# Kernel optimization log

Hardware: AMD Instinct MI355X
Metric: run time of the kernel (lower is better)

The kernel has to match this reference:

```python
import jax, jax.numpy as jnp
import numpy as np
from jax import lax

EPS = 1e-5      # BatchNorm1d default eps
SLOPE = 0.01    # LeakyReLU default negative_slope
DN = ('NCDHW', 'OIDHW', 'NCDHW')
PAD_31 = ((1, 1), (0, 0), (1, 1))   # kernel (3,1,3), padding (1,0,1)
PAD_13 = ((0, 0), (1, 1), (1, 1))   # kernel (1,3,3), padding (0,1,1)
PAD_P = ((1, 1), (1, 1), (1, 1))    # pool kernel 3, padding 1
STRIDE_P = (2, 2, 1)                # height_pooling=False -> stride (2,2,1)


def setup_inputs() -> dict:
    key = jax.random.key(0)
    ks = jax.random.split(key, 8)
    B, Cin, Cout = 1, 32, 64
    D1, D2, D3 = 160, 160, 32
    mask = jax.random.randint(ks[0], (B, 1, D1, D2, D3), 0, 2) > 0
    x = jax.random.normal(ks[1], (B, Cin, D1, D2, D3), dtype=jnp.float32)

    def w(k, cin, cout, kd, kh, kw):
        return jax.random.normal(k, (cout, cin, kd, kh, kw), dtype=jnp.float32) * 0.05

    inp = {
        'x': x, 'mask': mask,
        'W_A1': w(ks[2], Cin, Cout, 3, 1, 3),
        'W_A2': w(ks[3], Cout, Cout, 1, 3, 3),
        'W_B1': w(ks[4], Cin, Cout, 1, 3, 3),
        'W_B2': w(ks[5], Cout, Cout, 3, 1, 3),
        'W_pool': w(ks[6], Cout, Cout, 3, 3, 3),
    }
    for name in ('A1', 'A2', 'B1', 'B2'):
        inp['g_' + name] = jnp.ones((Cout,), jnp.float32)
        inp['b_' + name] = jnp.zeros((Cout,), jnp.float32)
    return inp


def _conv(h, W, pad, stride=(1, 1, 1)):
    return lax.conv_general_dilated(h, W, stride, pad, dimension_numbers=DN)


def _lrelu(h):
    return jnp.where(h >= 0, h, SLOPE * h)


def _masked_bn(h, m, n_active, gamma, beta):
    # BatchNorm1d over the [N_active, C] sparse feature tensor:
    # per-channel stats over active voxels only (biased variance, training mode).
    mean = jnp.sum(h * m, axis=(0, 2, 3, 4)) / n_active
    mu = mean[None, :, None, None, None]
    var = jnp.sum(((h - mu) ** 2) * m, axis=(0, 2, 3, 4)) / n_active
    inv = lax.rsqrt(var + EPS)[None, :, None, None, None]
    out = (h - mu) * inv * gamma[None, :, None, None, None] + beta[None, :, None, None, None]
    return out * m  # keep inactive sites exactly zero


def reference(x, mask, W_A1, W_A2, W_B1, W_B2, W_pool,
              g_A1, b_A1, g_A2, b_A2, g_B1, b_B1, g_B2, b_B2):
    m = mask.astype(x.dtype)                      # [B,1,D1,D2,D3] active-site indicator
    n_active = jnp.sum(m)
    xs = x * m                                    # sparse input: zero at inactive voxels

    def subm(h, W, pad):
        # submanifold conv: compute only at active output sites (same site set as input)
        return _conv(h, W, pad) * m

    # branch A: conv3x1 -> LeakyReLU -> BN -> conv1x3 -> LeakyReLU -> BN
    res_A = _masked_bn(_lrelu(subm(xs, W_A1, PAD_31)), m, n_active, g_A1, b_A1)
    res_A = _masked_bn(_lrelu(subm(res_A, W_A2, PAD_13)), m, n_active, g_A2, b_A2)

    # branch B: conv1x3 -> LeakyReLU -> BN -> conv3x1 -> LeakyReLU -> BN
    res_B = _masked_bn(_lrelu(subm(xs, W_B1, PAD_13)), m, n_active, g_B1, b_B1)
    res_B = _masked_bn(_lrelu(subm(res_B, W_B2, PAD_31)), m, n_active, g_B2, b_B2)

    res_B = res_B + res_A

    # strided SparseConv3d pool: output active where any input in 3x3x3 window is active
    ones_k = jnp.ones((1, 1, 3, 3, 3), x.dtype)
    out_mask = (_conv(m, ones_k, PAD_P, STRIDE_P) > 0).astype(x.dtype)
    down = _conv(res_B, W_pool, PAD_P, STRIDE_P) * out_mask
    return (down, res_B)
```

## Files before the change

### kernel.cpp

```cpp
#include <hip/hip_runtime.h>

static constexpr int ND1=160, ND2=160, ND3=32;
static constexpr int SP  = ND1*ND2*ND3;
static constexpr int CO  = 64;
static constexpr int OD1=80, OD2=80, OD3=32;
static constexpr int OSP = OD1*OD2*OD3;
static constexpr int NSC = 64;

typedef __attribute__((ext_vector_type(8))) short  short8;
typedef __attribute__((ext_vector_type(4))) float  f32x4;

__device__ __forceinline__ float b2f(unsigned u){ return __uint_as_float(u<<16); }
__device__ __forceinline__ unsigned short f2b(float f){
    unsigned u = __float_as_uint(f);
    u += 0x7fffu + ((u>>16)&1u);
    return (unsigned short)(u>>16);
}

__global__ void k_detect(const unsigned char* __restrict__ mb, int* __restrict__ flag)
{
    __shared__ int lf;
    if (threadIdx.x == 0) lf = 0;
    __syncthreads();
    int f = 0;
    for (int i = blockIdx.x*256 + threadIdx.x; i < SP; i += gridDim.x*256) {
        unsigned char b = mb[i];
        if (b > 1) f |= 4;
        if (b != 0 && (i & 3)) f |= 1;
    }
    if (f) atomicOr(&lf, f);
    __syncthreads();
    if (threadIdx.x == 0 && lf) atomicOr(flag, lf);
}

__global__ void k_mask(const void* __restrict__ mraw, const int* __restrict__ flag,
                       float* __restrict__ m, float* __restrict__ nactN)
{
    int i = blockIdx.x*256 + threadIdx.x;
    int f = *flag;
    float v;
    if (f & 4)      v = (reinterpret_cast<const float*>(mraw)[i] != 0.f) ? 1.f : 0.f;
    else if (f & 1) v = (reinterpret_cast<const unsigned char*>(mraw)[i] != 0) ? 1.f : 0.f;
    else            v = (reinterpret_cast<const int*>(mraw)[i] != 0) ? 1.f : 0.f;
    m[i] = v;
    float s = v;
    #pragma unroll
    for (int off = 32; off > 0; off >>= 1) s += __shfl_xor(s, off);
    __shared__ float wsum[4];
    if ((threadIdx.x & 63) == 0) wsum[threadIdx.x >> 6] = s;
    __syncthreads();
    if (threadIdx.x == 0) atomicAdd(&nactN[blockIdx.x & (NSC-1)], wsum[0]+wsum[1]+wsum[2]+wsum[3]);
}

__global__ void k_outmask(const float* __restrict__ m, float* __restrict__ om)
{
    int i = blockIdx.x*256 + threadIdx.x;
    int o3 = i & 31; int t = i >> 5; int o2 = t % OD2; int o1 = t / OD2;
    float s = 0.f;
    for (int kd = 0; kd < 3; kd++) { int d1 = 2*o1 - 1 + kd; if ((unsigned)d1 >= ND1) continue;
      for (int kh = 0; kh < 3; kh++) { int d2 = 2*o2 - 1 + kh; if ((unsigned)d2 >= ND2) continue;
        for (int kw = 0; kw < 3; kw++) { int d3 = o3 - 1 + kw; if ((unsigned)d3 >= ND3) continue;
          s += m[(d1*ND2 + d2)*ND3 + d3];
        } } }
    om[i] = (s > 0.f) ? 1.f : 0.f;
}

__global__ void k_finalize2(const float* __restrict__ SN0, const float* __restrict__ g0,
                            const float* __restrict__ b0, float* __restrict__ o0,
                            const float* __restrict__ SN1, const float* __restrict__ g1,
                            const float* __restrict__ b1, float* __restrict__ o1,
                            const float* __restrict__ nactN)
{
    const float* SN = blockIdx.x ? SN1 : SN0;
    const float* g  = blockIdx.x ? g1  : g0;
    const float* b  = blockIdx.x ? b1  : b0;
    float*       o  = blockIdx.x ? o1  : o0;
    int c = threadIdx.x;
    float s1 = 0.f, s2 = 0.f;
    #pragma unroll 4
    for (int k = 0; k < NSC; k++){
        s1 += SN[k*128 + c];
        s2 += SN[k*128 + 64 + c];
    }
    float nn = nactN[c];
    #pragma unroll
    for (int off = 32; off > 0; off >>= 1) nn += __shfl_xor(nn, off);
    float mean = s1 / nn;
    float var  = s2 / nn - mean*mean;
    float inv  = rsqrtf(var + 1e-5f);
    float sc   = inv * g[c];
    o[c]      = sc;
    o[64 + c] = b[c] - mean*sc;
}

__global__ void k_wprep(const float* __restrict__ W, unsigned short* __restrict__ Wt,
                        int CIN, int NT)
{
    int i = blockIdx.x*256 + threadIdx.x;
    int K = CIN*NT;
    if (i >= 64*K) return;
    int ksub = i & 31;
    int t = i >> 5;
    int co = t & 63;
    int kc = t >> 6;
    int nch = CIN >> 5;
    int tap = kc / nch;
    int ci  = (kc - tap*nch)*32 + ksub;
    Wt[i] = f2b(W[((size_t)co*CIN + ci)*NT + tap]);
}

__global__ void k_prep_x(const float* __restrict__ x, const float* __restrict__ m,
                         unsigned short* __restrict__ xt)
{
    __shared__ float t[64][33];
    int sp0 = blockIdx.x*64;
    int tid = threadIdx.x;
    int c = tid>>6, s = tid&63;
    float mm = m[sp0+s];
    #pragma unroll
    for (int r=0;r<8;r++){
        int ci = c + r*4;
        t[s][ci] = x[(size_t)ci*SP + sp0 + s]*mm;
    }
    __syncthreads();
    int sp = tid>>2, c0 = (tid&3)*8;
    unsigned short o[8];
    #pragma unroll
    for (int i=0;i<8;i++) o[i] = f2b(t[sp][c0+i]);
    uint4 pk;
    pk.x = o[0] | ((unsigned)o[1]<<16);
    pk.y = o[2] | ((unsigned)o[3]<<16);
    pk.z = o[4] | ((unsigned)o[5]<<16);
    pk.w = o[6] | ((unsigned)o[7]<<16);
    *reinterpret_cast<uint4*>(xt + (size_t)(sp0+sp)*32 + c0) = pk;
}

__global__ void k_resB(const unsigned short* __restrict__ hA, const unsigned short* __restrict__ hB,
                       const float* __restrict__ sA, const float* __restrict__ sB,
                       const float* __restrict__ m,
                       unsigned short* __restrict__ rbt, float* __restrict__ resf)
{
    __shared__ float t[64][65];
    __shared__ float ss[256];
    int tid = threadIdx.x;
    if (tid < 128){ ss[tid] = sA[tid]; ss[128+tid] = sB[tid]; }
    __syncthreads();
    int sp0 = blockIdx.x*64;
    int sp = tid>>2, c0 = (tid&3)*16;
    float mm = m[sp0+sp];
    const size_t base = (size_t)(sp0+sp)*64 + c0;
    uint4 a0 = *reinterpret_cast<const uint4*>(hA + base);
    uint4 a1 = *reinterpret_cast<const uint4*>(hA + base + 8);
    uint4 b0 = *reinterpret_cast<const uint4*>(hB + base);
    uint4 b1 = *reinterpret_cast<const uint4*>(hB + base + 8);
    unsigned ua[16] = {a0.x&0xffffu,a0.x>>16,a0.y&0xffffu,a0.y>>16,a0.z&0xffffu,a0.z>>16,a0.w&0xffffu,a0.w>>16,
                       a1.x&0xffffu,a1.x>>16,a1.y&0xffffu,a1.y>>16,a1.z&0xffffu,a1.z>>16,a1.w&0xffffu,a1.w>>16};
    unsigned ub[16] = {b0.x&0xffffu,b0.x>>16,b0.y&0xffffu,b0.y>>16,b0.z&0xffffu,b0.z>>16,b0.w&0xffffu,b0.w>>16,
                       b1.x&0xffffu,b1.x>>16,b1.y&0xffffu,b1.y>>16,b1.z&0xffffu,b1.z>>16,b1.w&0xffffu,b1.w>>16};
    unsigned short o[16];
    #pragma unroll
    for (int q=0;q<16;q++){
        int ci = c0+q;
        float v = (b2f(ua[q])*ss[ci] + ss[64+ci] + b2f(ub[q])*ss[128+ci] + ss[192+ci])*mm;
        t[sp][ci] = v;
        o[q] = f2b(v);
    }
    uint4 p0, p1;
    p0.x = o[0]|((unsigned)o[1]<<16);  p0.y = o[2]|((unsigned)o[3]<<16);
    p0.z = o[4]|((unsigned)o[5]<<16);  p0.w = o[6]|((unsigned)o[7]<<16);
    p1.x = o[8]|((unsigned)o[9]<<16);  p1.y = o[10]|((unsigned)o[11]<<16);
    p1.z = o[12]|((unsigned)o[13]<<16); p1.w = o[14]|((unsigned)o[15]<<16);
    *reinterpret_cast<uint4*>(rbt + base)     = p0;
    *reinterpret_cast<uint4*>(rbt + base + 8) = p1;
    __syncthreads();
    int ci = tid>>2, s0 = (tid&3)*16;
    #pragma unroll
    for (int kq=0;kq<4;kq++){
        float4 ov;
        ov.x = t[s0+4*kq+0][ci]; ov.y = t[s0+4*kq+1][ci];
        ov.z = t[s0+4*kq+2][ci]; ov.w = t[s0+4*kq+3][ci];
        *reinterpret_cast<float4*>(resf + (size_t)ci*SP + sp0 + s0 + 4*kq) = ov;
    }
}

template<int KIND, int CIN, bool HASAFF>
__launch_bounds__(256, (CIN==32) ? 3 : 2)
__global__ void mconv10(const unsigned short* __restrict__ in,
                        const unsigned short* __restrict__ Wt,
                        const float* __restrict__ scsh,
                        const float* __restrict__ mstage,
                        const float* __restrict__ mout,
                        unsigned short* __restrict__ outb,
                        float* __restrict__ statsN)
{
    constexpr int NCH  = CIN/32;
    constexpr int NKC  = NCH*9;
    constexpr int NR   = 10;
    constexpr int ROWB = 34*CIN*2;
    constexpr int SWZ  = (CIN==64) ? 7 : 3;
    __shared__ __align__(16) char lds[NR*ROWB];
    __shared__ float sst[128];

    const int tid = threadIdx.x;
    const int w = tid>>6, l = tid&63, g = l>>4, lj = l&15;
    const int h = w&1, rg = w>>1;

    int gi = (blockIdx.x & 7)*(gridDim.x>>3) + (blockIdx.x>>3);
    int z  = gi % 160;
    int r0 = (gi / 160)*8;

    if (tid < 128) sst[tid] = 0.f;

    const int sd3 = tid>>3;
    const int k0  = (tid&7)*(CIN/8);

    float sc[8], sh[8];
    if (HASAFF){
        #pragma unroll
        for (int j=0;j<8;j++){ sc[j]=scsh[k0+j]; sh[j]=scsh[64+k0+j]; }
    }

    for (int i = tid; i < NR*2*(CIN/8); i += 256){
        int per = CIN/8;
        int rr = i / (2*per);
        int rem = i - rr*2*per;
        int slot = (rem >= per) ? 33 : 0;
        int kc16 = (rem >= per) ? (rem - per) : rem;
        int dst = rr*ROWB + slot*CIN*2 + kc16*16;
        dst ^= ((slot&SWZ)<<4);
        *reinterpret_cast<uint4*>(lds + dst) = make_uint4(0,0,0,0);
    }

    if (CIN==64){
        uint4 v[NR]; float mmr[NR];
        #pragma unroll
        for (int rr=0; rr<NR; rr++){
            int rw = r0 - 1 + rr;
            v[rr] = make_uint4(0,0,0,0); mmr[rr] = 0.f;
            if ((unsigned)rw < 160u){
                int vox = (KIND==0) ? ((rw*ND2 + z)*ND3 + sd3)
                                    : ((z*ND2 + rw)*ND3 + sd3);
                v[rr] = *reinterpret_cast<const uint4*>(in + (size_t)vox*CIN + k0);
                if (HASAFF) mmr[rr] = mstage[vox];
            }
        }
        #pragma unroll
        for (int rr=0; rr<NR; rr++){
            uint4 vv = v[rr];
            if (HASAFF){
                float mm = mmr[rr];
                unsigned us[8] = {vv.x&0xffffu,vv.x>>16,vv.y&0xffffu,vv.y>>16,
                                  vv.z&0xffffu,vv.z>>16,vv.w&0xffffu,vv.w>>16};
                unsigned short o[8];
                #pragma unroll
                for (int j=0;j<8;j++) o[j] = f2b((b2f(us[j])*sc[j]+sh[j])*mm);
                vv.x = o[0]|((unsigned)o[1]<<16); vv.y = o[2]|((unsigned)o[3]<<16);
                vv.z = o[4]|((unsigned)o[5]<<16); vv.w = o[6]|((unsigned)o[7]<<16);
            }
            int dst = (rr*ROWB + (((sd3+1)*CIN + k0)*2)) ^ (((sd3+1)&SWZ)<<4);
            *reinterpret_cast<uint4*>(lds + dst) = vv;
        }
    } else {
        uint2 v[NR];
        #pragma unroll
        for (int rr=0; rr<NR; rr++){
            int rw = r0 - 1 + rr;
            v[rr] = make_uint2(0,0);
            if ((unsigned)rw < 160u){
                int vox = (KIND==0) ? ((rw*ND2 + z)*ND3 + sd3)
                                    : ((z*ND2 + rw)*ND3 + sd3);
                v[rr] = *reinterpret_cast<const uint2*>(in + (size_t)vox*CIN + k0);
            }
        }
        #pragma unroll
        for (int rr=0; rr<NR; rr++){
            int dst = (rr*ROWB + (((sd3+1)*CIN + k0)*2)) ^ (((sd3+1)&SWZ)<<4);
            *reinterpret_cast<uint2*>(lds + dst) = v[rr];
        }
    }

    short8 pa[NKC][2];
    {
        const unsigned short* wb = Wt + (size_t)(h*32)*32 + lj*32 + g*8;
        #pragma unroll
        for (int kc=0; kc<NKC; kc++){
            pa[kc][0] = *reinterpret_cast<const short8*>(wb + (size_t)kc*2048);
            pa[kc][1] = *reinterpret_cast<const short8*>(wb + (size_t)kc*2048 + 512);
        }
    }

    int tb[8], ovox[8];
    float mm[8];
    #pragma unroll
    for (int t=0;t<8;t++){
        int rowb = rg*4 + (t>>1);
        int o3   = (t&1)*16 + lj;
        tb[t] = rowb*ROWB + ((o3*CIN + g*8)*2);
        int o2r = r0 + rowb;
        ovox[t] = (KIND==0) ? ((o2r*ND2 + z)*ND3 + o3)
                            : ((z*ND2 + o2r)*ND3 + o3);
        mm[t] = mout[ovox[t]];
    }
    int swz[3];
    #pragma unroll
    for (int kw=0;kw<3;kw++) swz[kw] = ((lj+kw)&SWZ)<<4;

    __syncthreads();

    f32x4 acc[2][8];
    #pragma unroll
    for (int c=0;c<2;c++)
        #pragma unroll
        for (int t=0;t<8;t++)
            #pragma unroll
            for (int q=0;q<4;q++) acc[c][t][q] = 0.f;

    #pragma unroll
    for (int ch=0; ch<NCH; ch++){
        #pragma unroll
        for (int tap=0; tap<9; tap++){
            const int kd = tap/3, kw = tap - kd*3;
            const int kc = tap*NCH + ch;
            const int tapoff = kd*ROWB + (kw*CIN + ch*32)*2;
            #pragma unroll
            for (int t=0;t<8;t++){
                int off = (tb[t] + tapoff) ^ swz[kw];
                short8 bv = *reinterpret_cast<const short8*>(lds + off);
                acc[0][t] = __builtin_amdgcn_mfma_f32_16x16x32_bf16(pa[kc][0], bv, acc[0][t], 0,0,0);
                acc[1][t] = __builtin_amdgcn_mfma_f32_16x16x32_bf16(pa[kc][1], bv, acc[1][t], 0,0,0);
            }
        }
    }

    #pragma unroll
    for (int c=0;c<2;c++){
        const int ct = h*2 + c;
        float s1[4] = {0.f,0.f,0.f,0.f};
        float s2[4] = {0.f,0.f,0.f,0.f};
        #pragma unroll
        for (int t=0;t<8;t++){
            float v[4];
            #pragma unroll
            for (int r=0;r<4;r++){
                float xv = acc[c][t][r]*mm[t];
                xv = (xv >= 0.f) ? xv : 0.01f*xv;
                v[r] = xv; s1[r] += xv; s2[r] += xv*xv;
            }
            unsigned lo = f2b(v[0]) | ((unsigned)f2b(v[1])<<16);
            unsigned hi = f2b(v[2]) | ((unsigned)f2b(v[3])<<16);
            *reinterpret_cast<uint2*>(outb + (size_t)ovox[t]*64 + ct*16 + g*4) = make_uint2(lo,hi);
        }
        #pragma unroll
        for (int r=0;r<4;r++){
            float a = s1[r], b = s2[r];
            a += __shfl_xor(a,1); b += __shfl_xor(b,1);
            a += __shfl_xor(a,2); b += __shfl_xor(b,2);
            a += __shfl_xor(a,4); b += __shfl_xor(b,4);
            a += __shfl_xor(a,8); b += __shfl_xor(b,8);
            if (lj == 0){
                atomicAdd(&sst[ct*16 + g*4 + r], a);
                atomicAdd(&sst[64 + ct*16 + g*4 + r], b);
            }
        }
    }
    __syncthreads();
    if (tid < 128){
        float* sg = statsN + (size_t)(blockIdx.x & (NSC-1))*128;
        atomicAdd(&sg[tid], sst[tid]);
    }
}

__launch_bounds__(256, 4)
__global__ void mpool(const unsigned short* __restrict__ in,
                      const unsigned short* __restrict__ Wt,
                      const float* __restrict__ mout,
                      float* __restrict__ outf)
{
    constexpr int ROWB = 34*64*2;
    __shared__ __align__(16) char lds[9*ROWB];

    const int tid = threadIdx.x;
    const int w = tid>>6, l = tid&63, g = l>>4, lj = l&15;

    int gi = (blockIdx.x & 7)*(gridDim.x>>3) + (blockIdx.x>>3);
    int z  = gi % OD1;
    int r0 = (gi / OD1)*4;

    const int sd3 = tid>>3;
    const int k0  = (tid&7)*8;

    int swz[3];
    #pragma unroll
    for (int kw=0;kw<3;kw++) swz[kw] = ((lj+kw)&7)<<4;
    const int woff = lj*32 + g*8;

    for (int i = tid; i < 9*2*8; i += 256){
        int rr = i / 16;
        int rem = i - rr*16;
        int slot = (rem >= 8) ? 33 : 0;
        int kc16 = rem & 7;
        int dst = rr*ROWB + slot*128 + kc16*16;
        dst ^= ((slot&7)<<4);
        *reinterpret_cast<uint4*>(lds + dst) = make_uint4(0,0,0,0);
    }

    int tb2[2], ovx[2];
    float om[2];
    #pragma unroll
    for (int t=0;t<2;t++){
        int o3 = t*16 + lj;
        tb2[t] = (o3*64 + g*8)*2;
        ovx[t] = (z*OD2 + (r0 + w))*OD3 + o3;
        om[t]  = mout[ovx[t]];
    }
    f32x4 acc[4][2];
    #pragma unroll
    for (int a=0;a<4;a++)
        #pragma unroll
        for (int b=0;b<2;b++)
            #pragma unroll
            for (int q=0;q<4;q++) acc[a][b][q] = 0.f;

    short8 pa[2][4], pb[2][2];
    const int rrb = 2*w;

    uint4 rv[9];
    auto issue_plane = [&](int kd, uint4 (&dst)[9]){
        int d1 = 2*z - 1 + kd;
        bool pok = ((unsigned)d1 < (unsigned)ND1);
        #pragma unroll
        for (int rr=0; rr<9; rr++){
            int d2 = 2*r0 - 1 + rr;
            dst[rr] = make_uint4(0,0,0,0);
            if (pok && ((unsigned)d2 < (unsigned)ND2)){
                int vox = (d1*ND2 + d2)*ND3 + sd3;
                dst[rr] = *reinterpret_cast<const uint4*>(in + (size_t)vox*64 + k0);
            }
        }
    };

    #pragma unroll 1
    for (int kd=0; kd<3; kd++){
        issue_plane(kd, rv);
        __syncthreads();
        #pragma unroll
        for (int rr=0; rr<9; rr++){
            int dst = (rr*ROWB + (((sd3+1)*64 + k0)*2)) ^ (((sd3+1)&7)<<4);
            *reinterpret_cast<uint4*>(lds + dst) = rv[rr];
        }
        __syncthreads();

        auto loadA2 = [&](int tap, int ch, int buf){
            const int kh = tap/3, kw = tap - kh*3;
            const int kc = ((kd*3+kh)*3+kw)*2 + ch;
            const unsigned short* wp = Wt + (size_t)kc*2048 + woff;
            #pragma unroll
            for (int ct=0;ct<4;ct++) pa[buf][ct] = *reinterpret_cast<const short8*>(wp + ct*512);
        };
        auto loadB2 = [&](int tap, int ch, int buf){
            const int kh = tap/3, kw = tap - kh*3;
            const int tapoff = (rrb + kh)*ROWB + (kw*64 + ch*32)*2;
            #pragma unroll
            for (int t=0;t<2;t++){
                int off = (tb2[t] + tapoff) ^ swz[kw];
                pb[buf][t] = *reinterpret_cast<const short8*>(lds + off);
            }
        };

        #pragma unroll 1
        for (int ch=0; ch<2; ch++){
            loadA2(0, ch, 0); loadB2(0, ch, 0);
            #pragma unroll
            for (int tap=0; tap<9; tap++){
                const int cb = tap&1, nb = (tap&1)^1;
                if (tap < 8){ loadA2(tap+1, ch, nb); loadB2(tap+1, ch, nb); }
                #pragma unroll
                for (int t=0;t<2;t++)
                    #pragma unroll
                    for (int ct=0; ct<4; ct++)
                        acc[ct][t] = __builtin_amdgcn_mfma_f32_16x16x32_bf16(pa[cb][ct], pb[cb][t], acc[ct][t], 0,0,0);
            }
        }
    }
    #pragma unroll
    for (int t=0;t<2;t++){
        #pragma unroll
        for (int ct=0;ct<4;ct++){
            #pragma unroll
            for (int r=0;r<4;r++){
                int co = ct*16 + g*4 + r;
                outf[(size_t)co*OSP + ovx[t]] = acc[ct][t][r]*om[t];
            }
        }
    }
}

extern "C" void kernel_launch(void* const* d_in, const int* in_sizes, int n_in,
                              void* d_out, int out_size, void* d_ws, size_t ws_size,
                              hipStream_t stream)
{
    const float* x      = (const float*)d_in[0];
    const void*  mraw   = d_in[1];
    const float* W_A1   = (const float*)d_in[2];
    const float* W_A2   = (const float*)d_in[3];
    const float* W_B1   = (const float*)d_in[4];
    const float* W_B2   = (const float*)d_in[5];
    const float* W_pool = (const float*)d_in[6];
    const float* g_A1 = (const float*)d_in[7],  *b_A1 = (const float*)d_in[8];
    const float* g_A2 = (const float*)d_in[9],  *b_A2 = (const float*)d_in[10];
    const float* g_B1 = (const float*)d_in[11], *b_B1 = (const float*)d_in[12];
    const float* g_B2 = (const float*)d_in[13], *b_B2 = (const float*)d_in[14];

    char* p = (char*)d_ws;
    float* m     = (float*)p; p += (size_t)SP*4;
    float* omask = (float*)p; p += (size_t)OSP*4;
    float* statsN= (float*)p; p += 4*NSC*128*4;
    float* scsh  = (float*)p; p += 4*128*4;
    float* nactN = (float*)p; p += NSC*4;
    int*   flag  = (int*)p;   p += 4;
    p += 252;
    unsigned short* WtA1 = (unsigned short*)p; p += 288*64*2;
    unsigned short* WtA2 = (unsigned short*)p; p += 576*64*2;
    unsigned short* WtB1 = (unsigned short*)p; p += 288*64*2;
    unsigned short* WtB2 = (unsigned short*)p; p += 576*64*2;
    unsigned short* WtP  = (unsigned short*)p; p += 1728*64*2;
    unsigned short* X = (unsigned short*)p; p += (size_t)SP*32*2;
    unsigned short* P = (unsigned short*)p; p += (size_t)SP*64*2;
    unsigned short* Q = (unsigned short*)p; p += (size_t)SP*64*2;
    unsigned short* R = (unsigned short*)p; p += (size_t)SP*64*2;

    float* down = (float*)d_out;
    float* resf = down + (size_t)CO*OSP;

    hipMemsetAsync(statsN, 0, (4*NSC*128 + 4*128 + NSC)*4 + 4, stream);
    k_detect<<<256, 256, 0, stream>>>((const unsigned char*)mraw, flag);
    k_mask<<<SP/256, 256, 0, stream>>>(mraw, flag, m, nactN);
    k_outmask<<<OSP/256, 256, 0, stream>>>(m, omask);
    k_prep_x<<<SP/64, 256, 0, stream>>>(x, m, X);

    k_wprep<<<(64*288+255)/256, 256, 0, stream>>>(W_A1, WtA1, 32, 9);
    k_wprep<<<(64*576+255)/256, 256, 0, stream>>>(W_A2, WtA2, 64, 9);
    k_wprep<<<(64*288+255)/256, 256, 0, stream>>>(W_B1, WtB1, 32, 9);
    k_wprep<<<(64*576+255)/256, 256, 0, stream>>>(W_B2, WtB2, 64, 9);
    k_wprep<<<(64*1728+255)/256, 256, 0, stream>>>(W_pool, WtP, 64, 27);

    float* SA1 = statsN + 0*NSC*128;
    float* SA2 = statsN + 1*NSC*128;
    float* SB1 = statsN + 2*NSC*128;
    float* SB2 = statsN + 3*NSC*128;

    mconv10<0,32,false><<<3200, 256, 0, stream>>>(X, WtA1, nullptr, nullptr, m, P, SA1);
    mconv10<1,32,false><<<3200, 256, 0, stream>>>(X, WtB1, nullptr, nullptr, m, Q, SB1);
    k_finalize2<<<2, 64, 0, stream>>>(SA1, g_A1, b_A1, scsh + 0,
                                      SB1, g_B1, b_B1, scsh + 256, nactN);
    mconv10<1,64,true><<<3200, 256, 0, stream>>>(P, WtA2, scsh + 0,   m, m, R, SA2);
    mconv10<0,64,true><<<3200, 256, 0, stream>>>(Q, WtB2, scsh + 256, m, m, P, SB2);
    k_finalize2<<<2, 64, 0, stream>>>(SA2, g_A2, b_A2, scsh + 128,
                                      SB2, g_B2, b_B2, scsh + 384, nactN);
    k_resB<<<SP/64, 256, 0, stream>>>(R, P, scsh + 128, scsh + 384, m, Q, resf);
    mpool<<<1600, 256, 0, stream>>>(Q, WtP, omask, down);
}
```

Before: 674.2 us.

## Re-split pool conv warps by output-channel half and preload weights per plane

The strided pool convolution kernel changes its warp work split. Each warp now owns half of the output channels (2 channel tiles) across 2 output rows and 32 columns, instead of all 64 channels for one row. All 18 weight fragments for a depth plane are preloaded into registers alongside the global input loads, so weight fetches overlap the LDS staging and no longer sit inside the MFMA loop. The cost is much higher register use, so launch bounds drop from 4 to 2 blocks per CU, which lowers occupancy.

```diff
diff --git a/kernel.cpp b/kernel.cpp
--- a/kernel.cpp
+++ b/kernel.cpp
@@ -370,17 +370,18 @@
     }
 }
 
-__launch_bounds__(256, 4)
-__global__ void mpool(const unsigned short* __restrict__ in,
-                      const unsigned short* __restrict__ Wt,
-                      const float* __restrict__ mout,
-                      float* __restrict__ outf)
+__launch_bounds__(256, 2)
+__global__ void mpool3(const unsigned short* __restrict__ in,
+                       const unsigned short* __restrict__ Wt,
+                       const float* __restrict__ mout,
+                       float* __restrict__ outf)
 {
     constexpr int ROWB = 34*64*2;
     __shared__ __align__(16) char lds[9*ROWB];
 
     const int tid = threadIdx.x;
     const int w = tid>>6, l = tid&63, g = l>>4, lj = l&15;
+    const int h = w&1, rg = w>>1;
 
     int gi = (blockIdx.x & 7)*(gridDim.x>>3) + (blockIdx.x>>3);
     int z  = gi % OD1;
@@ -392,7 +393,6 @@
     int swz[3];
     #pragma unroll
     for (int kw=0;kw<3;kw++) swz[kw] = ((lj+kw)&7)<<4;
-    const int woff = lj*32 + g*8;
 
     for (int i = tid; i < 9*2*8; i += 256){
         int rr = i / 16;
@@ -404,44 +404,52 @@
         *reinterpret_cast<uint4*>(lds + dst) = make_uint4(0,0,0,0);
     }
 
-    int tb2[2], ovx[2];
-    float om[2];
-    #pragma unroll
-    for (int t=0;t<2;t++){
-        int o3 = t*16 + lj;
-        tb2[t] = (o3*64 + g*8)*2;
-        ovx[t] = (z*OD2 + (r0 + w))*OD3 + o3;
+    int tbl[4], ovx[4];
+    float om[4];
+    #pragma unroll
+    for (int t=0;t<4;t++){
+        int row = rg*2 + (t>>1);
+        int o3  = (t&1)*16 + lj;
+        tbl[t] = (o3*64 + g*8)*2;
+        ovx[t] = (z*OD2 + (r0 + row))*OD3 + o3;
         om[t]  = mout[ovx[t]];
     }
-    f32x4 acc[4][2];
-    #pragma unroll
-    for (int a=0;a<4;a++)
-        #pragma unroll
-        for (int b=0;b<2;b++)
-            #pragma unroll
-            for (int q=0;q<4;q++) acc[a][b][q] = 0.f;
-
-    short8 pa[2][4], pb[2][2];
-    const int rrb = 2*w;
+
+    f32x4 acc[2][4];
+    #pragma unroll
+    for (int c=0;c<2;c++)
+        #pragma unroll
+        for (int t=0;t<4;t++)
+            #pragma unroll
+            for (int q=0;q<4;q++) acc[c][t][q] = 0.f;
+
+    const unsigned short* wb = Wt + (size_t)(h*32)*32 + lj*32 + g*8;
 
     uint4 rv[9];
-    auto issue_plane = [&](int kd, uint4 (&dst)[9]){
-        int d1 = 2*z - 1 + kd;
-        bool pok = ((unsigned)d1 < (unsigned)ND1);
-        #pragma unroll
-        for (int rr=0; rr<9; rr++){
-            int d2 = 2*r0 - 1 + rr;
-            dst[rr] = make_uint4(0,0,0,0);
-            if (pok && ((unsigned)d2 < (unsigned)ND2)){
-                int vox = (d1*ND2 + d2)*ND3 + sd3;
-                dst[rr] = *reinterpret_cast<const uint4*>(in + (size_t)vox*64 + k0);
-            }
-        }
-    };
+    short8 pa[18][2];
 
     #pragma unroll 1
     for (int kd=0; kd<3; kd++){
-        issue_plane(kd, rv);
+        {
+            int d1 = 2*z - 1 + kd;
+            bool pok = ((unsigned)d1 < (unsigned)ND1);
+            #pragma unroll
+            for (int rr=0; rr<9; rr++){
+                int d2 = 2*r0 - 1 + rr;
+                rv[rr] = make_uint4(0,0,0,0);
+                if (pok && ((unsigned)d2 < (unsigned)ND2)){
+                    int vox = (d1*ND2 + d2)*ND3 + sd3;
+                    rv[rr] = *reinterpret_cast<const uint4*>(in + (size_t)vox*64 + k0);
+                }
+            }
+        }
+        #pragma unroll
+        for (int i=0;i<18;i++){
+            const int ch = i/9, tap = i - (i/9)*9;
+            const int kc = (kd*9 + tap)*2 + ch;
+            pa[i][0] = *reinterpret_cast<const short8*>(wb + (size_t)kc*2048);
+            pa[i][1] = *reinterpret_cast<const short8*>(wb + (size_t)kc*2048 + 512);
+        }
         __syncthreads();
         #pragma unroll
         for (int rr=0; rr<9; rr++){
@@ -449,47 +457,32 @@
             *reinterpret_cast<uint4*>(lds + dst) = rv[rr];
         }
         __syncthreads();
-
-        auto loadA2 = [&](int tap, int ch, int buf){
-            const int kh = tap/3, kw = tap - kh*3;
-            const int kc = ((kd*3+kh)*3+kw)*2 + ch;
-            const unsigned short* wp = Wt + (size_t)kc*2048 + woff;
-            #pragma unroll
-            for (int ct=0;ct<4;ct++) pa[buf][ct] = *reinterpret_cast<const short8*>(wp + ct*512);
-        };
-        auto loadB2 = [&](int tap, int ch, int buf){
-            const int kh = tap/3, kw = tap - kh*3;
-            const int tapoff = (rrb + kh)*ROWB + (kw*64 + ch*32)*2;
-            #pragma unroll
-            for (int t=0;t<2;t++){
-                int off = (tb2[t] + tapoff) ^ swz[kw];
-                pb[buf][t] = *reinterpret_cast<const short8*>(lds + off);
-            }
-        };
-
-        #pragma unroll 1
+        #pragma unroll
         for (int ch=0; ch<2; ch++){
-            loadA2(0, ch, 0); loadB2(0, ch, 0);
             #pragma unroll
             for (int tap=0; tap<9; tap++){
-                const int cb = tap&1, nb = (tap&1)^1;
-                if (tap < 8){ loadA2(tap+1, ch, nb); loadB2(tap+1, ch, nb); }
+                const int kh = tap/3, kw = tap - (tap/3)*3;
+                const int pi = ch*9 + tap;
                 #pragma unroll
-                for (int t=0;t<2;t++)
-                    #pragma unroll
-                    for (int ct=0; ct<4; ct++)
-                        acc[ct][t] = __builtin_amdgcn_mfma_f32_16x16x32_bf16(pa[cb][ct], pb[cb][t], acc[ct][t], 0,0,0);
-            }
-        }
-    }
-    #pragma unroll
-    for (int t=0;t<2;t++){
-        #pragma unroll
-        for (int ct=0;ct<4;ct++){
+                for (int t=0;t<4;t++){
+                    const int rowl = 2*(rg*2 + (t>>1)) + kh;
+                    int off = (rowl*ROWB + (kw*64 + ch*32)*2 + tbl[t]) ^ swz[kw];
+                    short8 bv = *reinterpret_cast<const short8*>(lds + off);
+                    acc[0][t] = __builtin_amdgcn_mfma_f32_16x16x32_bf16(pa[pi][0], bv, acc[0][t], 0,0,0);
+                    acc[1][t] = __builtin_amdgcn_mfma_f32_16x16x32_bf16(pa[pi][1], bv, acc[1][t], 0,0,0);
+                }
+            }
+        }
+    }
+    #pragma unroll
+    for (int c=0;c<2;c++){
+        const int ct = h*2 + c;
+        #pragma unroll
+        for (int t=0;t<4;t++){
             #pragma unroll
             for (int r=0;r<4;r++){
                 int co = ct*16 + g*4 + r;
-                outf[(size_t)co*OSP + ovx[t]] = acc[ct][t][r]*om[t];
+                outf[(size_t)co*OSP + ovx[t]] = acc[c][t][r]*om[t];
             }
         }
     }
@@ -558,5 +551,5 @@
     k_finalize2<<<2, 64, 0, stream>>>(SA2, g_A2, b_A2, scsh + 128,
                                       SB2, g_B2, b_B2, scsh + 384, nactN);
     k_resB<<<SP/64, 256, 0, stream>>>(R, P, scsh + 128, scsh + 384, m, Q, resf);
-    mpool<<<1600, 256, 0, stream>>>(Q, WtP, omask, down);
-}
+    mpool3<<<1600, 256, 0, stream>>>(Q, WtP, omask, down);
+}
```

Result: slower. 699.4 us (+3.7%).
